# Optimization experiments

Measured on AMD Instinct MI355X. Metric: run time of the kernel, lower is better.

The kernel has to match this reference:

```python
import jax, jax.numpy as jnp
import numpy as np

N = 100000
E = 1600000
F_IN = 64
F_OUT = 64
K = 3


def setup_inputs() -> dict:
    key = jax.random.key(0)
    k1, k2, k3, k4, k5 = jax.random.split(key, 5)
    x = jax.random.normal(k1, (N, F_IN), dtype=jnp.float32)
    rows = jnp.sort(jax.random.randint(k2, (E,), 0, N, dtype=jnp.int32))
    cols = jax.random.randint(k3, (E,), 0, N, dtype=jnp.int32)
    vals = jax.random.uniform(k4, (E,), dtype=jnp.float32)
    # xavier-uniform-ish weights
    limit = float(np.sqrt(6.0 / (F_IN + F_OUT)))
    weight = jax.random.uniform(k5, (K, F_IN, F_OUT), dtype=jnp.float32,
                                minval=-limit, maxval=limit)
    bias = jnp.zeros((F_OUT,), dtype=jnp.float32)
    return {"x": x, "rows": rows, "cols": cols, "vals": vals,
            "weight": weight, "bias": bias}


def _spmm(vals, rows, cols, h):
    # adj @ h with adj in COO form: out[i] = sum_{e: rows[e]==i} vals[e] * h[cols[e]]
    return jax.ops.segment_sum(vals[:, None] * h[cols], rows, num_segments=N)


def reference(x, rows, cols, vals, weight, bias):
    Tx_0 = x                              # T_0(L) x = x
    Tx_1 = _spmm(vals, rows, cols, x)     # T_1(L) x = L x
    out = Tx_0 @ weight[0] + Tx_1 @ weight[1]
    for k in range(2, K):                 # Chebyshev recurrence (K is small/static)
        Tx_2 = 2.0 * _spmm(vals, rows, cols, Tx_1) - Tx_0
        out = out + Tx_2 @ weight[k]
        Tx_0, Tx_1 = Tx_1, Tx_2
    return out + bias
```

## Files before the change

kernel.cpp:

```cpp
#include <hip/hip_runtime.h>

constexpr int NN = 100000;
constexpr int NE = 1600000;
constexpr int F  = 64;

typedef short bf16x8 __attribute__((ext_vector_type(8)));
typedef float f32x4  __attribute__((ext_vector_type(4)));

__device__ __forceinline__ float bf_lo(unsigned u) { return __uint_as_float(u << 16); }
__device__ __forceinline__ float bf_hi(unsigned u) { return __uint_as_float(u & 0xFFFF0000u); }
__device__ __forceinline__ unsigned pack_bf16(float a, float b) {
    unsigned ua = __float_as_uint(a);
    unsigned ub = __float_as_uint(b);
    ua = (ua + 0x7FFFu + ((ua >> 16) & 1u)) >> 16;
    ub = (ub + 0x7FFFu + ((ub >> 16) & 1u)) & 0xFFFF0000u;
    return ua | ub;
}

constexpr int B_CVT = NN * F / 8 / 256;
constexpr int B_RP  = NE / 256;
constexpr int B_W   = 192 * 64 / 256;

__global__ __launch_bounds__(256)
void prep_k(const float* __restrict__ x, ushort* __restrict__ xb,
            const int* __restrict__ rows, int* __restrict__ row_ptr,
            const float* __restrict__ w, ushort* __restrict__ wt) {
    const int b = blockIdx.x;
    if (b < B_CVT) {
        int tid = b * 256 + threadIdx.x;
        const float4* p = (const float4*)x + (size_t)tid * 2;
        float4 a = p[0], c = p[1];
        uint4 o = make_uint4(pack_bf16(a.x, a.y), pack_bf16(a.z, a.w),
                             pack_bf16(c.x, c.y), pack_bf16(c.z, c.w));
        ((uint4*)xb)[tid] = o;
    } else if (b < B_CVT + B_RP) {
        int e = (b - B_CVT) * 256 + threadIdx.x;
        int r1 = rows[e];
        int r2 = (e == NE - 1) ? NN : rows[e + 1];
        for (int r = r1 + 1; r <= r2; ++r) row_ptr[r] = e + 1;
        if (e == 0)
            for (int r = 0; r <= r1; ++r) row_ptr[r] = 0;
    } else {
        int tid = (b - B_CVT - B_RP) * 256 + threadIdx.x;
        int k = tid >> 6, n = tid & 63;
        unsigned u = __float_as_uint(w[tid]);
        u = (u + 0x7FFFu + ((u >> 16) & 1u)) >> 16;
        wt[n * 192 + k] = (ushort)u;
    }
}

template<bool SECOND>
__global__ __launch_bounds__(256)
void spmm_k(const int* __restrict__ row_ptr, const int* __restrict__ cols,
            const float* __restrict__ vals, const ushort* __restrict__ src,
            const ushort* __restrict__ x0, ushort* __restrict__ dst) {
    const int lane = threadIdx.x & 63;
    const int fgrp = lane & 7;
    const int g    = lane >> 3;
    const int r    = (blockIdx.x * 4 + (threadIdx.x >> 6)) * 8 + g;
    const int e0 = row_ptr[r];
    const int e1 = row_ptr[r + 1];
    const int deg = e1 - e0;
    int maxdeg = deg;
    maxdeg = max(maxdeg, __shfl_xor(maxdeg, 8));
    maxdeg = max(maxdeg, __shfl_xor(maxdeg, 16));
    maxdeg = max(maxdeg, __shfl_xor(maxdeg, 32));

    float acc[8] = {};
    #pragma unroll 2
    for (int s = 0; s < maxdeg; ++s) {
        const bool act = s < deg;
        int ec = act ? (e0 + s) : (e1 - 1);
        ec = ec < 0 ? 0 : ec;
        const int   cj = cols[ec];
        const float vv = vals[ec];
        const float vj = act ? vv : 0.f;
        uint4 raw = *(const uint4*)(src + (size_t)cj * F + fgrp * 8);
        acc[0] += vj * bf_lo(raw.x); acc[1] += vj * bf_hi(raw.x);
        acc[2] += vj * bf_lo(raw.y); acc[3] += vj * bf_hi(raw.y);
        acc[4] += vj * bf_lo(raw.z); acc[5] += vj * bf_hi(raw.z);
        acc[6] += vj * bf_lo(raw.w); acc[7] += vj * bf_hi(raw.w);
    }

    float o[8];
    if (SECOND) {
        uint4 xr = *(const uint4*)(x0 + (size_t)r * F + fgrp * 8);
        o[0] = 2.f * acc[0] - bf_lo(xr.x); o[1] = 2.f * acc[1] - bf_hi(xr.x);
        o[2] = 2.f * acc[2] - bf_lo(xr.y); o[3] = 2.f * acc[3] - bf_hi(xr.y);
        o[4] = 2.f * acc[4] - bf_lo(xr.z); o[5] = 2.f * acc[5] - bf_hi(xr.z);
        o[6] = 2.f * acc[6] - bf_lo(xr.w); o[7] = 2.f * acc[7] - bf_hi(xr.w);
    } else {
        #pragma unroll
        for (int t = 0; t < 8; ++t) o[t] = acc[t];
    }
    uint4 ov = make_uint4(pack_bf16(o[0], o[1]), pack_bf16(o[2], o[3]),
                          pack_bf16(o[4], o[5]), pack_bf16(o[6], o[7]));
    *(uint4*)(dst + (size_t)r * F + fgrp * 8) = ov;
}

__global__ __launch_bounds__(256)
void dense_k(const ushort* __restrict__ xb, const ushort* __restrict__ t1,
             const ushort* __restrict__ t2, const ushort* __restrict__ wt,
             const float* __restrict__ bias, float* __restrict__ out) {
    __shared__ float lds[4][16 * 68];
    const int tid  = threadIdx.x;
    const int lane = tid & 63;
    const int wv   = tid >> 6;
    const int row0 = blockIdx.x * 64 + wv * 16;
    const int m    = lane & 15;
    const int quad = lane >> 4;
    int arow = row0 + m;
    if (arow >= NN) arow = NN - 1;

    f32x4 acc[4] = {};
    #pragma unroll
    for (int kb = 0; kb < 6; ++kb) {
        const int kbase = kb * 32;
        const ushort* seg = (kb < 2) ? xb : (kb < 4) ? t1 : t2;
        const int off = (kbase & 63) + quad * 8;
        bf16x8 a = *(const bf16x8*)(seg + (size_t)arow * F + off);
        #pragma unroll
        for (int t = 0; t < 4; ++t) {
            const int n = t * 16 + m;
            bf16x8 b = *(const bf16x8*)(wt + (size_t)n * 192 + kbase + quad * 8);
            acc[t] = __builtin_amdgcn_mfma_f32_16x16x32_bf16(a, b, acc[t], 0, 0, 0);
        }
    }

    float* sl = lds[wv];
    #pragma unroll
    for (int t = 0; t < 4; ++t) {
        const float bv = bias[t * 16 + m];
        #pragma unroll
        for (int rr = 0; rr < 4; ++rr)
            sl[(quad * 4 + rr) * 68 + t * 16 + m] = acc[t][rr] + bv;
    }
    __syncthreads();
    const int m4 = (lane & 15) * 4;
    #pragma unroll
    for (int p = 0; p < 4; ++p) {
        const int rl = p * 4 + (lane >> 4);
        const int grow = row0 + rl;
        f32x4 v = *(const f32x4*)(sl + rl * 68 + m4);
        if (grow < NN)
            *(f32x4*)(out + (size_t)grow * F + m4) = v;
    }
}

extern "C" void kernel_launch(void* const* d_in, const int* in_sizes, int n_in,
                              void* d_out, int out_size, void* d_ws, size_t ws_size,
                              hipStream_t stream) {
    const float* x    = (const float*)d_in[0];
    const int*   rows = (const int*)  d_in[1];
    const int*   cols = (const int*)  d_in[2];
    const float* vals = (const float*)d_in[3];
    const float* w    = (const float*)d_in[4];
    const float* bias = (const float*)d_in[5];
    float* out = (float*)d_out;

    char* ws = (char*)d_ws;
    int* row_ptr = (int*)ws;
    size_t off = (((size_t)(NN + 1) * sizeof(int)) + 255) & ~(size_t)255;
    ushort* xb  = (ushort*)(ws + off);
    ushort* t1b = xb  + (size_t)NN * F;
    ushort* t2b = t1b + (size_t)NN * F;
    ushort* wt  = t2b + (size_t)NN * F;

    prep_k<<<B_CVT + B_RP + B_W, 256, 0, stream>>>(x, xb, rows, row_ptr, w, wt);
    spmm_k<false><<<NN / 32, 256, 0, stream>>>(row_ptr, cols, vals, xb,  nullptr, t1b);
    spmm_k<true ><<<NN / 32, 256, 0, stream>>>(row_ptr, cols, vals, t1b, xb,      t2b);
    dense_k<<<(NN + 63) / 64, 256, 0, stream>>>(xb, t1b, t2b, wt, bias, out);
}
```

Before: 186.0 us.

## Slice SpMM features per XCD and interleave cols/vals into packed edge array

Packs cols and vals into a single int2 edge array during prep so each edge needs one load. Restructures the SpMM grid so each XCD (derived from blockIdx mod 8) handles a 16-feature slice of the source matrix, shrinking the gathered working set per XCD so it fits better in that XCD's L2. Each lane now covers 8 features of one row, with 2 lanes per row, so every row's edge list is read four times across slices. This trades more edge-index traffic and a longer per-thread loop for better cache locality on the random gathers. It relies on the round-robin block-to-XCD dispatch, which is not guaranteed.

```diff
diff --git a/kernel.cpp b/kernel.cpp
--- a/kernel.cpp
+++ b/kernel.cpp
@@ -24,6 +24,8 @@
 __global__ __launch_bounds__(256)
 void prep_k(const float* __restrict__ x, ushort* __restrict__ xb,
             const int* __restrict__ rows, int* __restrict__ row_ptr,
+            const int* __restrict__ cols, const float* __restrict__ vals,
+            int2* __restrict__ ev,
             const float* __restrict__ w, ushort* __restrict__ wt) {
     const int b = blockIdx.x;
     if (b < B_CVT) {
@@ -35,6 +37,7 @@
         ((uint4*)xb)[tid] = o;
     } else if (b < B_CVT + B_RP) {
         int e = (b - B_CVT) * 256 + threadIdx.x;
+        ev[e] = make_int2(cols[e], __float_as_int(vals[e]));
         int r1 = rows[e];
         int r2 = (e == NE - 1) ? NN : rows[e + 1];
         for (int r = r1 + 1; r <= r2; ++r) row_ptr[r] = e + 1;
@@ -49,53 +52,67 @@
     }
 }
 
+constexpr int B_SPMM = 8 * 391;
+
 template<bool SECOND>
 __global__ __launch_bounds__(256)
-void spmm_k(const int* __restrict__ row_ptr, const int* __restrict__ cols,
-            const float* __restrict__ vals, const ushort* __restrict__ src,
-            const ushort* __restrict__ x0, ushort* __restrict__ dst) {
+void spmm_k(const int* __restrict__ row_ptr, const int2* __restrict__ ev,
+            const ushort* __restrict__ src, const ushort* __restrict__ x0,
+            ushort* __restrict__ dst) {
+    const int bid   = blockIdx.x;
+    const int xcd   = bid & 7;
+    const int slice = xcd >> 1;
+    const int par   = xcd & 1;
+    const int j     = bid >> 3;
+    const int rowbase = (j * 2 + par) * 128;
     const int lane = threadIdx.x & 63;
-    const int fgrp = lane & 7;
-    const int g    = lane >> 3;
-    const int r    = (blockIdx.x * 4 + (threadIdx.x >> 6)) * 8 + g;
-    const int e0 = row_ptr[r];
-    const int e1 = row_ptr[r + 1];
-    const int deg = e1 - e0;
+    const int wv   = threadIdx.x >> 6;
+    const int fgrp = lane & 1;
+    const int rr   = lane >> 1;
+    const int r    = rowbase + wv * 32 + rr;
+    const int rc   = min(r, NN - 1);
+    const int e0 = row_ptr[rc];
+    const int e1 = row_ptr[rc + 1];
+    const int deg = (r < NN) ? (e1 - e0) : 0;
     int maxdeg = deg;
+    maxdeg = max(maxdeg, __shfl_xor(maxdeg, 2));
+    maxdeg = max(maxdeg, __shfl_xor(maxdeg, 4));
     maxdeg = max(maxdeg, __shfl_xor(maxdeg, 8));
     maxdeg = max(maxdeg, __shfl_xor(maxdeg, 16));
     maxdeg = max(maxdeg, __shfl_xor(maxdeg, 32));
+    const int elast = max(e1 - 1, 0);
+    const int soff  = slice * 16 + fgrp * 8;
 
     float acc[8] = {};
     #pragma unroll 2
     for (int s = 0; s < maxdeg; ++s) {
         const bool act = s < deg;
-        int ec = act ? (e0 + s) : (e1 - 1);
-        ec = ec < 0 ? 0 : ec;
-        const int   cj = cols[ec];
-        const float vv = vals[ec];
-        const float vj = act ? vv : 0.f;
-        uint4 raw = *(const uint4*)(src + (size_t)cj * F + fgrp * 8);
+        const int ec = act ? (e0 + s) : elast;
+        const int2 e = ev[ec];
+        const float vj = act ? __int_as_float(e.y) : 0.f;
+        uint4 raw = *(const uint4*)(src + (size_t)e.x * F + soff);
         acc[0] += vj * bf_lo(raw.x); acc[1] += vj * bf_hi(raw.x);
         acc[2] += vj * bf_lo(raw.y); acc[3] += vj * bf_hi(raw.y);
         acc[4] += vj * bf_lo(raw.z); acc[5] += vj * bf_hi(raw.z);
         acc[6] += vj * bf_lo(raw.w); acc[7] += vj * bf_hi(raw.w);
     }
 
-    float o[8];
-    if (SECOND) {
-        uint4 xr = *(const uint4*)(x0 + (size_t)r * F + fgrp * 8);
-        o[0] = 2.f * acc[0] - bf_lo(xr.x); o[1] = 2.f * acc[1] - bf_hi(xr.x);
-        o[2] = 2.f * acc[2] - bf_lo(xr.y); o[3] = 2.f * acc[3] - bf_hi(xr.y);
-        o[4] = 2.f * acc[4] - bf_lo(xr.z); o[5] = 2.f * acc[5] - bf_hi(xr.z);
-        o[6] = 2.f * acc[6] - bf_lo(xr.w); o[7] = 2.f * acc[7] - bf_hi(xr.w);
-    } else {
-        #pragma unroll
-        for (int t = 0; t < 8; ++t) o[t] = acc[t];
+    if (r < NN) {
+        float o[8];
+        if (SECOND) {
+            uint4 xr = *(const uint4*)(x0 + (size_t)r * F + soff);
+            o[0] = 2.f * acc[0] - bf_lo(xr.x); o[1] = 2.f * acc[1] - bf_hi(xr.x);
+            o[2] = 2.f * acc[2] - bf_lo(xr.y); o[3] = 2.f * acc[3] - bf_hi(xr.y);
+            o[4] = 2.f * acc[4] - bf_lo(xr.z); o[5] = 2.f * acc[5] - bf_hi(xr.z);
+            o[6] = 2.f * acc[6] - bf_lo(xr.w); o[7] = 2.f * acc[7] - bf_hi(xr.w);
+        } else {
+            #pragma unroll
+            for (int t = 0; t < 8; ++t) o[t] = acc[t];
+        }
+        uint4 ov = make_uint4(pack_bf16(o[0], o[1]), pack_bf16(o[2], o[3]),
+                              pack_bf16(o[4], o[5]), pack_bf16(o[6], o[7]));
+        *(uint4*)(dst + (size_t)r * F + soff) = ov;
     }
-    uint4 ov = make_uint4(pack_bf16(o[0], o[1]), pack_bf16(o[2], o[3]),
-                          pack_bf16(o[4], o[5]), pack_bf16(o[6], o[7]));
-    *(uint4*)(dst + (size_t)r * F + fgrp * 8) = ov;
 }
 
 __global__ __launch_bounds__(256)
@@ -165,9 +182,13 @@
     ushort* t1b = xb  + (size_t)NN * F;
     ushort* t2b = t1b + (size_t)NN * F;
     ushort* wt  = t2b + (size_t)NN * F;
+    char* evb = (char*)(wt + (size_t)64 * 192);
+    evb = (char*)(((size_t)evb + 255) & ~(size_t)255);
+    int2* ev = (int2*)evb;
 
-    prep_k<<<B_CVT + B_RP + B_W, 256, 0, stream>>>(x, xb, rows, row_ptr, w, wt);
-    spmm_k<false><<<NN / 32, 256, 0, stream>>>(row_ptr, cols, vals, xb,  nullptr, t1b);
-    spmm_k<true ><<<NN / 32, 256, 0, stream>>>(row_ptr, cols, vals, t1b, xb,      t2b);
+    prep_k<<<B_CVT + B_RP + B_W, 256, 0, stream>>>(x, xb, rows, row_ptr,
+                                                   cols, vals, ev, w, wt);
+    spmm_k<false><<<B_SPMM, 256, 0, stream>>>(row_ptr, ev, xb,  nullptr, t1b);
+    spmm_k<true ><<<B_SPMM, 256, 0, stream>>>(row_ptr, ev, t1b, xb,      t2b);
     dense_k<<<(NN + 63) / 64, 256, 0, stream>>>(xb, t1b, t2b, wt, bias, out);
 }
```

New measurement: 541.2 us. +191.0%, slower.

## Interleave cols/vals into int2 array and software-prefetch edge data in SpMM

Applied to the files above, without the earlier changes.

The prep kernel now packs cols and vals into one interleaved int2 edge array, so each SpMM iteration does one 8-byte load instead of two separate loads. The SpMM loop is rewritten to process two edges per step and load the next pair of edge entries while the current gathers are consumed, so the dependent cols→src load chain is pipelined. The cost is an extra write of the edge array in prep (12.8 MB) and extra register pressure.

```diff
diff --git a/kernel.cpp b/kernel.cpp
--- a/kernel.cpp
+++ b/kernel.cpp
@@ -24,6 +24,8 @@
 __global__ __launch_bounds__(256)
 void prep_k(const float* __restrict__ x, ushort* __restrict__ xb,
             const int* __restrict__ rows, int* __restrict__ row_ptr,
+            const int* __restrict__ cols, const float* __restrict__ vals,
+            int2* __restrict__ ev,
             const float* __restrict__ w, ushort* __restrict__ wt) {
     const int b = blockIdx.x;
     if (b < B_CVT) {
@@ -35,6 +37,7 @@
         ((uint4*)xb)[tid] = o;
     } else if (b < B_CVT + B_RP) {
         int e = (b - B_CVT) * 256 + threadIdx.x;
+        ev[e] = make_int2(cols[e], __float_as_int(vals[e]));
         int r1 = rows[e];
         int r2 = (e == NE - 1) ? NN : rows[e + 1];
         for (int r = r1 + 1; r <= r2; ++r) row_ptr[r] = e + 1;
@@ -51,9 +54,9 @@
 
 template<bool SECOND>
 __global__ __launch_bounds__(256)
-void spmm_k(const int* __restrict__ row_ptr, const int* __restrict__ cols,
-            const float* __restrict__ vals, const ushort* __restrict__ src,
-            const ushort* __restrict__ x0, ushort* __restrict__ dst) {
+void spmm_k(const int* __restrict__ row_ptr, const int2* __restrict__ ev,
+            const ushort* __restrict__ src, const ushort* __restrict__ x0,
+            ushort* __restrict__ dst) {
     const int lane = threadIdx.x & 63;
     const int fgrp = lane & 7;
     const int g    = lane >> 3;
@@ -65,21 +68,39 @@
     maxdeg = max(maxdeg, __shfl_xor(maxdeg, 8));
     maxdeg = max(maxdeg, __shfl_xor(maxdeg, 16));
     maxdeg = max(maxdeg, __shfl_xor(maxdeg, 32));
+    const int elast = max(e1 - 1, 0);
+
+    int2 eq0, eq1;
+    {
+        const int ec0 = (0 < deg) ? e0 : elast;
+        const int ec1 = (1 < deg) ? (e0 + 1) : elast;
+        eq0 = ev[ec0]; eq1 = ev[ec1];
+        if (!(0 < deg)) eq0.y = 0;
+        if (!(1 < deg)) eq1.y = 0;
+    }
 
     float acc[8] = {};
-    #pragma unroll 2
-    for (int s = 0; s < maxdeg; ++s) {
-        const bool act = s < deg;
-        int ec = act ? (e0 + s) : (e1 - 1);
-        ec = ec < 0 ? 0 : ec;
-        const int   cj = cols[ec];
-        const float vv = vals[ec];
-        const float vj = act ? vv : 0.f;
-        uint4 raw = *(const uint4*)(src + (size_t)cj * F + fgrp * 8);
-        acc[0] += vj * bf_lo(raw.x); acc[1] += vj * bf_hi(raw.x);
-        acc[2] += vj * bf_lo(raw.y); acc[3] += vj * bf_hi(raw.y);
-        acc[4] += vj * bf_lo(raw.z); acc[5] += vj * bf_hi(raw.z);
-        acc[6] += vj * bf_lo(raw.w); acc[7] += vj * bf_hi(raw.w);
+    for (int s = 0; s < maxdeg; s += 2) {
+        uint4 raw0 = *(const uint4*)(src + (size_t)eq0.x * F + fgrp * 8);
+        uint4 raw1 = *(const uint4*)(src + (size_t)eq1.x * F + fgrp * 8);
+        const int s2 = s + 2, s3 = s + 3;
+        const int ec2 = (s2 < deg) ? (e0 + s2) : elast;
+        const int ec3 = (s3 < deg) ? (e0 + s3) : elast;
+        int2 en0 = ev[ec2];
+        int2 en1 = ev[ec3];
+        if (!(s2 < deg)) en0.y = 0;
+        if (!(s3 < deg)) en1.y = 0;
+        const float v0 = __int_as_float(eq0.y);
+        const float v1 = __int_as_float(eq1.y);
+        acc[0] += v0 * bf_lo(raw0.x); acc[1] += v0 * bf_hi(raw0.x);
+        acc[2] += v0 * bf_lo(raw0.y); acc[3] += v0 * bf_hi(raw0.y);
+        acc[4] += v0 * bf_lo(raw0.z); acc[5] += v0 * bf_hi(raw0.z);
+        acc[6] += v0 * bf_lo(raw0.w); acc[7] += v0 * bf_hi(raw0.w);
+        acc[0] += v1 * bf_lo(raw1.x); acc[1] += v1 * bf_hi(raw1.x);
+        acc[2] += v1 * bf_lo(raw1.y); acc[3] += v1 * bf_hi(raw1.y);
+        acc[4] += v1 * bf_lo(raw1.z); acc[5] += v1 * bf_hi(raw1.z);
+        acc[6] += v1 * bf_lo(raw1.w); acc[7] += v1 * bf_hi(raw1.w);
+        eq0 = en0; eq1 = en1;
     }
 
     float o[8];
@@ -165,9 +186,13 @@
     ushort* t1b = xb  + (size_t)NN * F;
     ushort* t2b = t1b + (size_t)NN * F;
     ushort* wt  = t2b + (size_t)NN * F;
+    char* evb = (char*)(wt + (size_t)64 * 192);
+    evb = (char*)(((size_t)evb + 255) & ~(size_t)255);
+    int2* ev = (int2*)evb;
 
-    prep_k<<<B_CVT + B_RP + B_W, 256, 0, stream>>>(x, xb, rows, row_ptr, w, wt);
-    spmm_k<false><<<NN / 32, 256, 0, stream>>>(row_ptr, cols, vals, xb,  nullptr, t1b);
-    spmm_k<true ><<<NN / 32, 256, 0, stream>>>(row_ptr, cols, vals, t1b, xb,      t2b);
+    prep_k<<<B_CVT + B_RP + B_W, 256, 0, stream>>>(x, xb, rows, row_ptr,
+                                                   cols, vals, ev, w, wt);
+    spmm_k<false><<<NN / 32, 256, 0, stream>>>(row_ptr, ev, xb,  nullptr, t1b);
+    spmm_k<true ><<<NN / 32, 256, 0, stream>>>(row_ptr, ev, t1b, xb,      t2b);
     dense_k<<<(NN + 63) / 64, 256, 0, stream>>>(xb, t1b, t2b, wt, bias, out);
 }
```

Measured after the change: 190.6 us. 1.02x slower.
